# Kernel tuning notes

Hardware: AMD Instinct MI355X
Metric: run time of the kernel (lower is better)

## Reference

```python
import jax, jax.numpy as jnp
import numpy as np

SLOPE = 25.0  # snntorch surrogate.fast_sigmoid default slope
THR = 1.0
BETA = 0.5
NUM_HEADS = 8

@jax.custom_vjp
def spike(u):
    # forward: heaviside; backward: fast-sigmoid surrogate
    return (u > 0).astype(u.dtype)

def _spike_fwd(u):
    return (u > 0).astype(u.dtype), u

def _spike_bwd(u, g):
    return (g / (SLOPE * jnp.abs(u) + 1.0) ** 2,)

spike.defvjp(_spike_fwd, _spike_bwd)

def lif(inp, mem):
    # snntorch Leaky, reset_mechanism='subtract': reset from previous mem (detached)
    reset = jax.lax.stop_gradient((mem > THR).astype(mem.dtype))
    mem_new = BETA * mem + inp - reset * THR
    spk = spike(mem_new - THR)
    return spk, mem_new

def conv1x1(x, W):
    # nn.Conv2d(C,C,1,bias=False): pure channel matmul
    return jnp.einsum('bihw,oi->bohw', x, W)

def setup_inputs():
    key = jax.random.key(0)
    ks = jax.random.split(key, 5)
    B, C, H, W = 8, 256, 64, 64
    x = jax.random.normal(ks[0], (B, C, H, W), jnp.float32)
    z = jnp.zeros((B, C, H, W), jnp.float32)
    s = 1.0 / np.sqrt(C)
    Wq = jax.random.normal(ks[1], (C, C), jnp.float32) * s
    Wk = jax.random.normal(ks[2], (C, C), jnp.float32) * s
    Wv = jax.random.normal(ks[3], (C, C), jnp.float32) * s
    Wo = jax.random.normal(ks[4], (C, C), jnp.float32) * s
    gamma = jnp.ones((C,), jnp.float32)
    beta_bn = jnp.zeros((C,), jnp.float32)
    return {'x': x, 'q_mem': z, 'k_mem': z, 'v_mem': z,
            'Wq': Wq, 'Wk': Wk, 'Wv': Wv, 'Wo': Wo,
            'gamma': gamma, 'beta_bn': beta_bn}

def reference(x, q_mem, k_mem, v_mem, Wq, Wk, Wv, Wo, gamma, beta_bn):
    B, C, H, W = x.shape
    N = H * W
    hd = C // NUM_HEADS
    scale = hd ** -0.5

    q_spk, q_mem_n = lif(conv1x1(x, Wq), q_mem)
    k_spk, k_mem_n = lif(conv1x1(x, Wk), k_mem)
    v_spk, v_mem_n = lif(conv1x1(x, Wv), v_mem)

    # bipolar spikes in {-1,+1}, reshape to (B, h, N, d)
    def to_heads(s):
        t = (2.0 * s - 1.0).reshape(B, NUM_HEADS, hd, N)
        return jnp.transpose(t, (0, 1, 3, 2))

    q = jax.nn.elu(to_heads(q_spk)) + 1.0
    k = jax.nn.elu(to_heads(k_spk)) + 1.0
    v = to_heads(v_spk)

    kv = jnp.einsum('bhnd,bhne->bhde', k, v)            # (B,h,d,d)
    out = jnp.einsum('bhnd,bhde->bhne', q, kv) * scale  # (B,h,N,d)
    k_sum = jnp.sum(k, axis=2)                          # (B,h,d)
    denom = jnp.einsum('bhnd,bhd->bhn', q, k_sum) + 1e-6
    out = out / denom[..., None]

    out = jnp.transpose(out, (0, 1, 3, 2)).reshape(B, C, H, W)
    out = conv1x1(out, Wo)

    # BatchNorm2d, training mode (biased batch stats), eps=1e-5
    mean = jnp.mean(out, axis=(0, 2, 3), keepdims=True)
    var = jnp.var(out, axis=(0, 2, 3), keepdims=True)
    out = (out - mean) / jnp.sqrt(var + 1e-5)
    out = out * gamma[None, :, None, None] + beta_bn[None, :, None, None]

    return (out, q_mem_n, k_mem_n, v_mem_n)
```

## Files before the change

### kernel.cpp

```cpp
#include <hip/hip_runtime.h>

#define B_ 8
#define C_ 256
#define N_ 4096
#define HD_ 32

#define ALPHA_ 0.36787944117144233f
#define BETAS_ (2.0f - ALPHA_)
#define SCALE_ 0.17677669529663687f

typedef _Float16 f16;
typedef _Float16 f16x8 __attribute__((ext_vector_type(8)));
typedef float f32x4 __attribute__((ext_vector_type(4)));
typedef unsigned long long u64;
typedef __attribute__((address_space(3))) f16 lds_f16;

#define MFMA(a,b,c) __builtin_amdgcn_mfma_f32_16x16x32_f16((a),(b),(c),0,0,0)

#define GLDS(g, l) __builtin_amdgcn_global_load_lds( \
    (const __attribute__((address_space(1))) void*)(g), \
    (__attribute__((address_space(3))) void*)(l), 16, 0, 0)

#define DSR(dst, off) asm volatile("ds_read_b128 %0, %1" : "=v"(dst) : "v"(off))

#define GLA(dst, ptr, ofs) asm volatile( \
    "global_load_dwordx4 %0, %1, off offset:%c2" \
    : "=v"(dst) : "v"(ptr), "i"(ofs))

template<int N> __device__ __forceinline__ void wait_vmcnt() {
    if constexpr (N == 0)       asm volatile("s_waitcnt vmcnt(0)" ::: "memory");
    else if constexpr (N == 2)  asm volatile("s_waitcnt vmcnt(2)" ::: "memory");
    else if constexpr (N == 4)  asm volatile("s_waitcnt vmcnt(4)" ::: "memory");
    else if constexpr (N == 6)  asm volatile("s_waitcnt vmcnt(6)" ::: "memory");
    else if constexpr (N == 8)  asm volatile("s_waitcnt vmcnt(8)" ::: "memory");
    else if constexpr (N == 12) asm volatile("s_waitcnt vmcnt(12)" ::: "memory");
    else if constexpr (N == 16) asm volatile("s_waitcnt vmcnt(16)" ::: "memory");
}

__global__ __launch_bounds__(256) void transpose_split(
    const float* __restrict__ x, f16* __restrict__ XTh, f16* __restrict__ XTl)
{
    __shared__ float tile[32][257];
    int t = threadIdx.x;
    int b = blockIdx.z, i0 = blockIdx.y * 32, n0 = blockIdx.x * 256;
    const float* src = x + ((size_t)b * C_ + i0) * N_ + n0;
    int r = t >> 3, c0 = (t & 7) * 32;
    #pragma unroll
    for (int q = 0; q < 8; ++q) {
        float4 v = *reinterpret_cast<const float4*>(src + (size_t)r * N_ + c0 + q * 4);
        tile[r][c0 + q*4 + 0] = v.x; tile[r][c0 + q*4 + 1] = v.y;
        tile[r][c0 + q*4 + 2] = v.z; tile[r][c0 + q*4 + 3] = v.w;
    }
    __syncthreads();
    size_t ob = ((size_t)b * N_ + n0 + t) * C_ + i0;
    #pragma unroll
    for (int q = 0; q < 4; ++q) {
        f16x8 hv, lv;
        #pragma unroll
        for (int j = 0; j < 8; ++j) {
            float v = tile[q*8 + j][t];
            f16 h = (f16)v;
            hv[j] = h;
            lv[j] = (f16)(v - (float)h);
        }
        *reinterpret_cast<f16x8*>(XTh + ob + q*8) = hv;
        *reinterpret_cast<f16x8*>(XTl + ob + q*8) = lv;
    }
}

__global__ __launch_bounds__(256) void weight_split(
    const float* __restrict__ Wq, const float* __restrict__ Wk,
    const float* __restrict__ Wv, const float* __restrict__ Wo,
    f16* __restrict__ Wch, f16* __restrict__ Wcl)
{
    int idx4 = (blockIdx.x * 256 + threadIdx.x) * 4;
    int o = idx4 >> 8, i = idx4 & 255;
    const float* src = (o < 256) ? (Wq + (size_t)o * 256)
                     : (o < 512) ? (Wk + (size_t)(o - 256) * 256)
                     : (o < 768) ? (Wv + (size_t)(o - 512) * 256)
                                 : (Wo + (size_t)(o - 768) * 256);
    float4 v = *reinterpret_cast<const float4*>(src + i);
    f16 h0 = (f16)v.x, h1 = (f16)v.y, h2 = (f16)v.z, h3 = (f16)v.w;
    f16 hh[4] = { h0, h1, h2, h3 };
    f16 ll[4] = { (f16)(v.x - (float)h0), (f16)(v.y - (float)h1),
                  (f16)(v.z - (float)h2), (f16)(v.w - (float)h3) };
    *reinterpret_cast<uint2*>(Wch + idx4) = *reinterpret_cast<uint2*>(hh);
    *reinterpret_cast<uint2*>(Wcl + idx4) = *reinterpret_cast<uint2*>(ll);
}

template<bool LIF, bool FULLP>
__global__ __launch_bounds__(256, 2) void mfma_gemm(
    const f16* __restrict__ Wch, const f16* __restrict__ Wcl,
    const f16* __restrict__ Bh,  const f16* __restrict__ Bl,
    const float* __restrict__ mq, const float* __restrict__ mk2,
    const float* __restrict__ mv,
    float* __restrict__ o0, float* __restrict__ o1, float* __restrict__ o2,
    u64* __restrict__ rowAll)
{
    constexpr int SLOTS = FULLP ? 1024 : 512;
    constexpr int NGL   = FULLP ? 4 : 2;
    constexpr int NA    = FULLP ? 8 : 4;

    int gid = blockIdx.x;
    int b = gid & 7, slot = gid >> 3;
    int conv, oTi, nt;
    if (LIF) { conv = slot % 3; int rest = slot / 3; oTi = rest & 1; nt = rest >> 1; }
    else     { conv = 0;        oTi = slot & 1;      nt = slot >> 1; }
    int wRow0 = (LIF ? conv * 256 : 768) + oTi * 128;
    int chOut0 = oTi * 128;
    int nT = nt * 128;

    const float* memP = nullptr; float* outP; u64* rowP = nullptr;
    if (LIF) {
        memP = (conv == 0) ? mq : (conv == 1) ? mk2 : mv;
        outP = (conv == 0) ? o0 : (conv == 1) ? o1 : o2;
        rowP = rowAll + (size_t)conv * (8 * 256 * 64);
    } else outP = o0;

    __shared__ __align__(16) f16 smem[3][SLOTS * 8];

    int t = threadIdx.x;
    int wid = t >> 6, lane = t & 63;
    int wm = wid >> 1, wn = wid & 1;
    int lr = lane & 15, g = lane >> 4;

    const f16* gB[NGL];
    #pragma unroll
    for (int i = 0; i < NGL; ++i) {
        int s = i * 256 + t;
        int sp = s & 511;
        int r = sp >> 2, c = (sp & 3) ^ ((r >> 1) & 3);
        const f16* plane = (s < 512) ? Bh : Bl;
        gB[i] = plane + ((size_t)b * N_ + nT + r) * 256 + c * 8;
    }

    const f16* aPh[4]; const f16* aPl[4];
    #pragma unroll
    for (int m = 0; m < 4; ++m) {
        int off = (wRow0 + wm * 64 + m * 16 + lr) * 256 + g * 8;
        aPh[m] = Wch + off;
        aPl[m] = Wcl + off;
    }

    unsigned lbase = (unsigned)(size_t)(lds_f16*)&smem[0][0];
    unsigned offB[4];
    #pragma unroll
    for (int n = 0; n < 4; ++n) {
        int r = wn * 64 + n * 16 + lr;
        offB[n] = (unsigned)((r * 4 + (g ^ ((r >> 1) & 3))) * 16);
    }

    f32x4 acc[4][4];
    #pragma unroll
    for (int m = 0; m < 4; ++m)
        #pragma unroll
        for (int n = 0; n < 4; ++n) acc[m][n] = (f32x4){0.f, 0.f, 0.f, 0.f};

    f16x8 aH[2][4], aL[2][4];

    #pragma unroll
    for (int i = 0; i < NGL; ++i) GLDS(gB[i], &smem[0][(i * 256 + t) * 8]);
    #pragma unroll
    for (int m = 0; m < 4; ++m) {
        GLA(aH[0][m], aPh[m], 0);
        if (FULLP) GLA(aL[0][m], aPl[m], 0);
    }
    #pragma unroll
    for (int i = 0; i < NGL; ++i) GLDS(gB[i] + 32, &smem[1][(i * 256 + t) * 8]);
    wait_vmcnt<NGL>();
    __builtin_amdgcn_s_barrier();
    __builtin_amdgcn_sched_barrier(0);

#define GEMM_STEP(KS) do { \
    constexpr int ks = (KS); \
    constexpr int cur = ks & 1, nxt = (ks + 1) & 1; \
     \
    const unsigned base = lbase + (unsigned)((ks % 3) * (SLOTS * 16)); \
    f16x8 bhf[4], blf[4]; \
    _Pragma("unroll") \
    for (int n = 0; n < 4; ++n) { \
        DSR(bhf[n], base + offB[n]); \
        if (FULLP) DSR(blf[n], base + offB[n] + 8192); \
    } \
    __builtin_amdgcn_sched_barrier(0); \
     \
    if constexpr (ks < 7) { \
        _Pragma("unroll") \
        for (int m = 0; m < 4; ++m) { \
            GLA(aH[nxt][m], aPh[m], (ks + 1) * 64); \
            if (FULLP) GLA(aL[nxt][m], aPl[m], (ks + 1) * 64); \
        } \
    } \
    __builtin_amdgcn_sched_barrier(0); \
     \
    if constexpr (ks < 6) { \
        _Pragma("unroll") \
        for (int i = 0; i < NGL; ++i) \
            GLDS(gB[i] + (ks + 2) * 32, &smem[(ks + 2) % 3][(i * 256 + t) * 8]); \
    } \
    __builtin_amdgcn_sched_barrier(0); \
    asm volatile("s_waitcnt lgkmcnt(0)" ::: "memory"); \
    __builtin_amdgcn_sched_barrier(0); \
     \
    wait_vmcnt<(ks <= 5) ? (2 * NGL + NA) : (ks == 6 ? (NGL + NA) : 0)>(); \
    __builtin_amdgcn_sched_barrier(0); \
    _Pragma("unroll") \
    for (int n = 0; n < 4; ++n) \
        _Pragma("unroll") \
        for (int m = 0; m < 4; ++m) { \
            acc[m][n] = MFMA(aH[cur][m], bhf[n], acc[m][n]); \
            if (FULLP) { \
                acc[m][n] = MFMA(aH[cur][m], blf[n], acc[m][n]); \
                acc[m][n] = MFMA(aL[cur][m], bhf[n], acc[m][n]); \
            } \
        } \
    __builtin_amdgcn_sched_barrier(0); \
    if constexpr (ks < 7) { \
         \
        wait_vmcnt<(ks <= 5) ? (NA + NGL) : NA>(); \
        __builtin_amdgcn_s_barrier(); \
        __builtin_amdgcn_sched_barrier(0); \
    } \
} while (0)

    GEMM_STEP(0); GEMM_STEP(1); GEMM_STEP(2); GEMM_STEP(3);
    GEMM_STEP(4); GEMM_STEP(5); GEMM_STEP(6); GEMM_STEP(7);
#undef GEMM_STEP

    if (LIF) {
        #pragma unroll
        for (int m = 0; m < 4; ++m) {
            int oLoc = chOut0 + wm * 64 + m * 16 + g * 4;
            u64 rw0 = 0, rw1 = 0, rw2 = 0, rw3 = 0;
            #pragma unroll
            for (int n = 0; n < 4; ++n) {
                int nn = nT + wn * 64 + n * 16 + lr;
                #pragma unroll
                for (int r = 0; r < 4; ++r) {
                    size_t idx = ((size_t)b * C_ + oLoc + r) * N_ + nn;
                    float mm = memP[idx];
                    float v = 0.5f * mm + acc[m][n][r] - (mm > 1.0f ? 1.0f : 0.0f);
                    outP[idx] = v;
                    u64 bl = __ballot(v > 1.0f);
                    u64 fld = ((bl >> (g * 16)) & 0xFFFFull) << (n * 16);
                    if (r == 0) rw0 |= fld; else if (r == 1) rw1 |= fld;
                    else if (r == 2) rw2 |= fld; else rw3 |= fld;
                }
            }
            if (lr == 0) {
                size_t rb = ((size_t)b * 256 + oLoc) * 64 + (nt * 2 + wn);
                rowP[rb]       = rw0;
                rowP[rb + 64]  = rw1;
                rowP[rb + 128] = rw2;
                rowP[rb + 192] = rw3;
            }
        }
    } else {
        #pragma unroll
        for (int m = 0; m < 4; ++m) {
            int oLoc = chOut0 + wm * 64 + m * 16 + g * 4;
            #pragma unroll
            for (int n = 0; n < 4; ++n) {
                int nn = nT + wn * 64 + n * 16 + lr;
                #pragma unroll
                for (int r = 0; r < 4; ++r) {
                    size_t idx = ((size_t)b * C_ + oLoc + r) * N_ + nn;
                    outP[idx] = acc[m][n][r];
                }
            }
        }
    }
}

__global__ __launch_bounds__(256) void kv_stage1(
    const u64* __restrict__ krow, const u64* __restrict__ vrow,
    int* __restrict__ pkv, int* __restrict__ pck, int* __restrict__ pcv)
{
    int bh = blockIdx.x, sl = blockIdx.y;
    int b = bh >> 3, h = bh & 7;
    __shared__ u64 kr[32][9], vr[32][9];
    int t = threadIdx.x;
    {
        int d = t >> 3, w = t & 7;
        size_t a = ((size_t)b * 256 + h * HD_ + d) * 64 + sl * 8 + w;
        kr[d][w] = krow[a];
        vr[d][w] = vrow[a];
    }
    __syncthreads();

    int base = bh * 8 + sl;
    if (t < 32) {
        int c = 0;
        #pragma unroll
        for (int w = 0; w < 8; ++w) c += __popcll(kr[t][w]);
        pck[base * 32 + t] = c;
    } else if (t < 64) {
        int dd = t - 32, c = 0;
        #pragma unroll
        for (int w = 0; w < 8; ++w) c += __popcll(vr[dd][w]);
        pcv[base * 32 + dd] = c;
    }
    int d = t >> 3, e0 = (t & 7) * 4;
    #pragma unroll
    for (int j = 0; j < 4; ++j) {
        int e = e0 + j, P = 0;
        #pragma unroll
        for (int w = 0; w < 8; ++w) P += __popcll(kr[d][w] & vr[e][w]);
        pkv[(size_t)base * 1024 + d * 32 + e] = P;
    }
}

__global__ __launch_bounds__(256) void kv_stage2(
    const int* __restrict__ pkv, const int* __restrict__ pck,
    const int* __restrict__ pcv, float* __restrict__ kvp, float* __restrict__ ksump)
{
    int bh = blockIdx.x, t = threadIdx.x;
    __shared__ float ck[32], cv[32];
    if (t < 32) {
        int s = 0;
        #pragma unroll
        for (int sl = 0; sl < 8; ++sl) s += pck[(bh * 8 + sl) * 32 + t];
        ck[t] = (float)s;
    } else if (t < 64) {
        int dd = t - 32, s = 0;
        #pragma unroll
        for (int sl = 0; sl < 8; ++sl) s += pcv[(bh * 8 + sl) * 32 + dd];
        cv[dd] = (float)s;
    }
    __syncthreads();
    int d = t >> 3, e0 = (t & 7) * 4;
    #pragma unroll
    for (int j = 0; j < 4; ++j) {
        int e = e0 + j, P = 0;
        #pragma unroll
        for (int sl = 0; sl < 8; ++sl) P += pkv[(size_t)(bh * 8 + sl) * 1024 + d * 32 + e];
        float skv = 2.0f * (float)P - ck[d];
        float sv  = 2.0f * cv[e] - 4096.0f;
        kvp[(size_t)bh * 1024 + d * 32 + e] = ALPHA_ * sv + BETAS_ * skv;
    }
    if ((t & 7) == 0)
        ksump[bh * 32 + d] = ALPHA_ * 4096.0f + BETAS_ * ck[d];
}

__global__ __launch_bounds__(256) void att_kernel(
    const u64* __restrict__ qrow, const float* __restrict__ kvp,
    const float* __restrict__ ksump, f16* __restrict__ ATh)
{
    int bh = blockIdx.y; int b = bh >> 3, h = bh & 7;
    int n0 = blockIdx.x * 256;

    __shared__ u64 qw[32][5];
    int t = threadIdx.x;
    if (t < 128) {
        int d2 = t >> 2, w4 = t & 3;
        qw[d2][w4] = qrow[((size_t)b * 256 + h * HD_ + d2) * 64 + (n0 >> 6) + w4];
    }
    __syncthreads();

    float q[32];
    #pragma unroll
    for (int d2 = 0; d2 < 32; ++d2)
        q[d2] = ((qw[d2][t >> 6] >> (t & 63)) & 1) ? 2.0f : ALPHA_;

    const float* ksb = ksump + bh * 32;
    float den = 1e-6f;
    #pragma unroll
    for (int d2 = 0; d2 < 32; ++d2) den += q[d2] * ksb[d2];
    float rden = SCALE_ / den;

    const float* kvb = kvp + (size_t)bh * 1024;
    size_t ob = ((size_t)b * N_ + n0 + t) * C_ + h * HD_;
    #pragma unroll
    for (int qq = 0; qq < 4; ++qq) {
        f16x8 hv;
        #pragma unroll
        for (int j = 0; j < 8; ++j) {
            int e = qq * 8 + j;
            float num = 0.0f;
            #pragma unroll
            for (int d2 = 0; d2 < 32; ++d2) num += q[d2] * kvb[d2 * 32 + e];
            hv[j] = (f16)(num * rden);
        }
        *reinterpret_cast<f16x8*>(ATh + ob + qq * 8) = hv;
    }
}

__global__ __launch_bounds__(1024) void bn_stats(
    const float* __restrict__ out2, float* __restrict__ stats)
{
    int o = blockIdx.x, t = threadIdx.x;
    double s = 0.0, ss = 0.0;
    for (int b = 0; b < B_; ++b) {
        const float* p = out2 + ((size_t)b * C_ + o) * N_;
        float4 v = *reinterpret_cast<const float4*>(&p[t * 4]);
        s  += (double)v.x + (double)v.y + (double)v.z + (double)v.w;
        ss += (double)v.x * v.x + (double)v.y * v.y + (double)v.z * v.z + (double)v.w * v.w;
    }
    __shared__ double rs[1024], rss[1024];
    rs[t] = s; rss[t] = ss;
    __syncthreads();
    for (int st = 512; st > 0; st >>= 1) {
        if (t < st) { rs[t] += rs[t + st]; rss[t] += rss[t + st]; }
        __syncthreads();
    }
    if (t == 0) {
        double mean = rs[0] / 32768.0;
        double var  = rss[0] / 32768.0 - mean * mean;
        stats[o * 2 + 0] = (float)mean;
        stats[o * 2 + 1] = (float)(1.0 / sqrt(var + 1e-5));
    }
}

__global__ __launch_bounds__(256) void bn_apply(
    float* __restrict__ out, const float* __restrict__ stats,
    const float* __restrict__ gamma, const float* __restrict__ beta)
{
    size_t i = ((size_t)blockIdx.x * 256 + threadIdx.x) * 4;
    int o = (int)((i >> 12) & 255);
    float m = stats[o * 2], r = stats[o * 2 + 1];
    float g = gamma[o] * r;
    float c = beta[o] - m * g;
    float4 v = *reinterpret_cast<float4*>(&out[i]);
    v.x = v.x * g + c; v.y = v.y * g + c;
    v.z = v.z * g + c; v.w = v.w * g + c;
    *reinterpret_cast<float4*>(&out[i]) = v;
}

extern "C" void kernel_launch(void* const* d_in, const int* in_sizes, int n_in,
                              void* d_out, int out_size, void* d_ws, size_t ws_size,
                              hipStream_t stream)
{
    (void)in_sizes; (void)n_in; (void)out_size; (void)ws_size;

    const float* x     = (const float*)d_in[0];
    const float* qmem  = (const float*)d_in[1];
    const float* kmem  = (const float*)d_in[2];
    const float* vmem  = (const float*)d_in[3];
    const float* Wq    = (const float*)d_in[4];
    const float* Wk    = (const float*)d_in[5];
    const float* Wv    = (const float*)d_in[6];
    const float* Wo    = (const float*)d_in[7];
    const float* gamma = (const float*)d_in[8];
    const float* beta  = (const float*)d_in[9];

    const size_t TSZ = (size_t)B_ * C_ * N_;
    float* out0 = (float*)d_out;
    float* outq = out0 + TSZ;
    float* outk = outq + TSZ;
    float* outv = outk + TSZ;

    const size_t RSZ = (size_t)8 * 256 * 64;
    char* w = (char*)d_ws;
    f16* XTh = (f16*)w;           w += TSZ * 2;
    f16* XTl = (f16*)w;           w += TSZ * 2;
    f16* ATh = (f16*)w;           w += TSZ * 2;
    f16* Wch = (f16*)w;           w += 1024 * 256 * 2;
    f16* Wcl = (f16*)w;           w += 1024 * 256 * 2;
    u64* rowm = (u64*)w;          w += 3 * RSZ * 8;
    int* pkv = (int*)w;           w += 64 * 8 * 1024 * 4;
    int* pck = (int*)w;           w += 64 * 8 * 32 * 4;
    int* pcv = (int*)w;           w += 64 * 8 * 32 * 4;
    float* kvp   = (float*)w;     w += 64 * 1024 * 4;
    float* ksump = (float*)w;     w += 64 * 32 * 4;
    float* stats = (float*)w;     w += 256 * 2 * 4;

    dim3 blk(256);

    transpose_split<<<dim3(16, 8, 8), blk, 0, stream>>>(x, XTh, XTl);
    weight_split<<<dim3(256), blk, 0, stream>>>(Wq, Wk, Wv, Wo, Wch, Wcl);

    mfma_gemm<true, true><<<dim3(1536), blk, 0, stream>>>(
        Wch, Wcl, XTh, XTl, qmem, kmem, vmem, outq, outk, outv, rowm);

    kv_stage1<<<dim3(64, 8), blk, 0, stream>>>(rowm + RSZ, rowm + 2 * RSZ, pkv, pck, pcv);
    kv_stage2<<<dim3(64), blk, 0, stream>>>(pkv, pck, pcv, kvp, ksump);

    att_kernel<<<dim3(16, 64), blk, 0, stream>>>(rowm, kvp, ksump, ATh);

    mfma_gemm<false, false><<<dim3(512), blk, 0, stream>>>(
        Wch, Wcl, ATh, ATh, nullptr, nullptr, nullptr, out0, nullptr, nullptr, nullptr);

    bn_stats<<<dim3(256), dim3(1024), 0, stream>>>(out0, stats);
    bn_apply<<<dim3(8192), blk, 0, stream>>>(out0, stats, gamma, beta);
}
```

Measured before the change: 174.6 us.

## Fuse BN partial sums into output GEMM epilogue and merge KV stages

The output GEMM epilogue now computes per-channel partial sums and sums of squares with warp shuffles and writes them to a small partial buffer. bn_stats then reduces only these partials instead of rereading the full 32 MB output tensor. The two KV popcount kernels are merged into one kernel per batch-head, which drops a launch and the intermediate buffers but gives only 64 blocks. Partial sums are now accumulated in float rather than double, which may change BN statistic precision slightly.

```diff
diff --git a/kernel.cpp b/kernel.cpp
--- a/kernel.cpp
+++ b/kernel.cpp
@@ -95,7 +95,7 @@
     const float* __restrict__ mq, const float* __restrict__ mk2,
     const float* __restrict__ mv,
     float* __restrict__ o0, float* __restrict__ o1, float* __restrict__ o2,
-    u64* __restrict__ rowAll)
+    u64* __restrict__ rowAll, float2* __restrict__ part)
 {
     constexpr int SLOTS = FULLP ? 1024 : 512;
     constexpr int NGL   = FULLP ? 4 : 2;
@@ -258,82 +258,67 @@
     } else {
         #pragma unroll
         for (int m = 0; m < 4; ++m) {
-            int oLoc = chOut0 + wm * 64 + m * 16 + g * 4;
             #pragma unroll
-            for (int n = 0; n < 4; ++n) {
-                int nn = nT + wn * 64 + n * 16 + lr;
+            for (int r = 0; r < 4; ++r) {
+                int ch = chOut0 + wm * 64 + m * 16 + g * 4 + r;
+                float s1 = 0.f, s2 = 0.f;
                 #pragma unroll
-                for (int r = 0; r < 4; ++r) {
-                    size_t idx = ((size_t)b * C_ + oLoc + r) * N_ + nn;
-                    outP[idx] = acc[m][n][r];
+                for (int n = 0; n < 4; ++n) {
+                    int nn = nT + wn * 64 + n * 16 + lr;
+                    size_t idx = ((size_t)b * C_ + ch) * N_ + nn;
+                    float v = acc[m][n][r];
+                    outP[idx] = v;
+                    s1 += v; s2 += v * v;
                 }
+                #pragma unroll
+                for (int w = 1; w < 16; w <<= 1) {
+                    s1 += __shfl_xor(s1, w);
+                    s2 += __shfl_xor(s2, w);
+                }
+                if (lr == 0)
+                    part[((size_t)ch * 8 + b) * 64 + nt * 2 + wn] = make_float2(s1, s2);
             }
         }
     }
 }
 
-__global__ __launch_bounds__(256) void kv_stage1(
+__global__ __launch_bounds__(256) void kv_kernel(
     const u64* __restrict__ krow, const u64* __restrict__ vrow,
-    int* __restrict__ pkv, int* __restrict__ pck, int* __restrict__ pcv)
-{
-    int bh = blockIdx.x, sl = blockIdx.y;
+    float* __restrict__ kvp, float* __restrict__ ksump)
+{
+    int bh = blockIdx.x;
     int b = bh >> 3, h = bh & 7;
-    __shared__ u64 kr[32][9], vr[32][9];
+    __shared__ u64 kr[32][65], vr[32][65];
+    __shared__ float ck[32], cv[32];
     int t = threadIdx.x;
     {
-        int d = t >> 3, w = t & 7;
-        size_t a = ((size_t)b * 256 + h * HD_ + d) * 64 + sl * 8 + w;
-        kr[d][w] = krow[a];
-        vr[d][w] = vrow[a];
+        size_t base = ((size_t)b * 256 + h * HD_) * 64;
+        #pragma unroll
+        for (int j = 0; j < 8; ++j) {
+            int idx = t * 8 + j;
+            int d = idx >> 6, w = idx & 63;
+            kr[d][w] = krow[base + idx];
+            vr[d][w] = vrow[base + idx];
+        }
     }
     __syncthreads();
 
-    int base = bh * 8 + sl;
     if (t < 32) {
         int c = 0;
-        #pragma unroll
-        for (int w = 0; w < 8; ++w) c += __popcll(kr[t][w]);
-        pck[base * 32 + t] = c;
+        for (int w = 0; w < 64; ++w) c += __popcll(kr[t][w]);
+        ck[t] = (float)c;
     } else if (t < 64) {
         int dd = t - 32, c = 0;
-        #pragma unroll
-        for (int w = 0; w < 8; ++w) c += __popcll(vr[dd][w]);
-        pcv[base * 32 + dd] = c;
-    }
+        for (int w = 0; w < 64; ++w) c += __popcll(vr[dd][w]);
+        cv[dd] = (float)c;
+    }
+    __syncthreads();
+
     int d = t >> 3, e0 = (t & 7) * 4;
     #pragma unroll
     for (int j = 0; j < 4; ++j) {
         int e = e0 + j, P = 0;
-        #pragma unroll
-        for (int w = 0; w < 8; ++w) P += __popcll(kr[d][w] & vr[e][w]);
-        pkv[(size_t)base * 1024 + d * 32 + e] = P;
-    }
-}
-
-__global__ __launch_bounds__(256) void kv_stage2(
-    const int* __restrict__ pkv, const int* __restrict__ pck,
-    const int* __restrict__ pcv, float* __restrict__ kvp, float* __restrict__ ksump)
-{
-    int bh = blockIdx.x, t = threadIdx.x;
-    __shared__ float ck[32], cv[32];
-    if (t < 32) {
-        int s = 0;
-        #pragma unroll
-        for (int sl = 0; sl < 8; ++sl) s += pck[(bh * 8 + sl) * 32 + t];
-        ck[t] = (float)s;
-    } else if (t < 64) {
-        int dd = t - 32, s = 0;
-        #pragma unroll
-        for (int sl = 0; sl < 8; ++sl) s += pcv[(bh * 8 + sl) * 32 + dd];
-        cv[dd] = (float)s;
-    }
-    __syncthreads();
-    int d = t >> 3, e0 = (t & 7) * 4;
-    #pragma unroll
-    for (int j = 0; j < 4; ++j) {
-        int e = e0 + j, P = 0;
-        #pragma unroll
-        for (int sl = 0; sl < 8; ++sl) P += pkv[(size_t)(bh * 8 + sl) * 1024 + d * 32 + e];
+        for (int w = 0; w < 64; ++w) P += __popcll(kr[d][w] & vr[e][w]);
         float skv = 2.0f * (float)P - ck[d];
         float sv  = 2.0f * cv[e] - 4096.0f;
         kvp[(size_t)bh * 1024 + d * 32 + e] = ALPHA_ * sv + BETAS_ * skv;
@@ -385,21 +370,18 @@
     }
 }
 
-__global__ __launch_bounds__(1024) void bn_stats(
-    const float* __restrict__ out2, float* __restrict__ stats)
+__global__ __launch_bounds__(256) void bn_stats(
+    const float2* __restrict__ part, float* __restrict__ stats)
 {
     int o = blockIdx.x, t = threadIdx.x;
-    double s = 0.0, ss = 0.0;
-    for (int b = 0; b < B_; ++b) {
-        const float* p = out2 + ((size_t)b * C_ + o) * N_;
-        float4 v = *reinterpret_cast<const float4*>(&p[t * 4]);
-        s  += (double)v.x + (double)v.y + (double)v.z + (double)v.w;
-        ss += (double)v.x * v.x + (double)v.y * v.y + (double)v.z * v.z + (double)v.w * v.w;
-    }
-    __shared__ double rs[1024], rss[1024];
+    float2 a = part[(size_t)o * 512 + t];
+    float2 c = part[(size_t)o * 512 + 256 + t];
+    double s = (double)a.x + (double)c.x;
+    double ss = (double)a.y + (double)c.y;
+    __shared__ double rs[256], rss[256];
     rs[t] = s; rss[t] = ss;
     __syncthreads();
-    for (int st = 512; st > 0; st >>= 1) {
+    for (int st = 128; st > 0; st >>= 1) {
         if (t < st) { rs[t] += rs[t + st]; rss[t] += rss[t + st]; }
         __syncthreads();
     }
@@ -457,9 +439,7 @@
     f16* Wch = (f16*)w;           w += 1024 * 256 * 2;
     f16* Wcl = (f16*)w;           w += 1024 * 256 * 2;
     u64* rowm = (u64*)w;          w += 3 * RSZ * 8;
-    int* pkv = (int*)w;           w += 64 * 8 * 1024 * 4;
-    int* pck = (int*)w;           w += 64 * 8 * 32 * 4;
-    int* pcv = (int*)w;           w += 64 * 8 * 32 * 4;
+    float2* part = (float2*)w;    w += 256 * 8 * 64 * 8;
     float* kvp   = (float*)w;     w += 64 * 1024 * 4;
     float* ksump = (float*)w;     w += 64 * 32 * 4;
     float* stats = (float*)w;     w += 256 * 2 * 4;
@@ -470,16 +450,16 @@
     weight_split<<<dim3(256), blk, 0, stream>>>(Wq, Wk, Wv, Wo, Wch, Wcl);
 
     mfma_gemm<true, true><<<dim3(1536), blk, 0, stream>>>(
-        Wch, Wcl, XTh, XTl, qmem, kmem, vmem, outq, outk, outv, rowm);
-
-    kv_stage1<<<dim3(64, 8), blk, 0, stream>>>(rowm + RSZ, rowm + 2 * RSZ, pkv, pck, pcv);
-    kv_stage2<<<dim3(64), blk, 0, stream>>>(pkv, pck, pcv, kvp, ksump);
+        Wch, Wcl, XTh, XTl, qmem, kmem, vmem, outq, outk, outv, rowm, nullptr);
+
+    kv_kernel<<<dim3(64), blk, 0, stream>>>(rowm + RSZ, rowm + 2 * RSZ, kvp, ksump);
 
     att_kernel<<<dim3(16, 64), blk, 0, stream>>>(rowm, kvp, ksump, ATh);
 
     mfma_gemm<false, false><<<dim3(512), blk, 0, stream>>>(
-        Wch, Wcl, ATh, ATh, nullptr, nullptr, nullptr, out0, nullptr, nullptr, nullptr);
-
-    bn_stats<<<dim3(256), dim3(1024), 0, stream>>>(out0, stats);
+        Wch, Wcl, ATh, ATh, nullptr, nullptr, nullptr, out0, nullptr, nullptr,
+        nullptr, part);
+
+    bn_stats<<<dim3(256), blk, 0, stream>>>(part, stats);
     bn_apply<<<dim3(8192), blk, 0, stream>>>(out0, stats, gamma, beta);
 }
```

New measurement: 177.7 us. No clear change (+1.8%).
